# Kernel optimization log

Measured on AMD Instinct MI355X. Metric: run time of the kernel, lower is better.

## Reference

```python
import jax, jax.numpy as jnp
import numpy as np
import math

D = 128  # hidden_dim
N_USERS = 10000
N_ITEMS = 12000
NEG_INF = -9e15


def setup_inputs() -> dict:
    key = jax.random.key(0)
    k1, k2, k3, k4, k5 = jax.random.split(key, 5)
    ufea = jax.random.normal(k1, (N_USERS, D), dtype=jnp.float32)
    inter = jax.random.normal(k2, (N_ITEMS, D), dtype=jnp.float32)
    adj = jax.random.randint(k3, (N_USERS, N_ITEMS), 0, 2, dtype=jnp.int32)
    # linear layer params (torch default init approximated with scaled normals)
    W = jax.random.normal(k4, (D, D), dtype=jnp.float32) / jnp.sqrt(jnp.float32(D))
    b = jax.random.normal(k5, (D,), dtype=jnp.float32) * 0.01
    return {"ufea": ufea, "inter": inter, "adj": adj, "W": W, "b": b}


def _leaky_relu2(x):
    # nn.LeakyReLU(2): negative_slope = 2
    return jnp.where(x > 0, x, 2.0 * x)


def reference(ufea, inter, adj, W, b):
    # GAT.forward_user with dropout in eval mode (identity).
    # Attention.forward(a=ufea, b=inter, adj)
    query = ufea @ W.T + b                      # [N, D]  nn.Linear
    scale = 1.0 / math.sqrt(D)
    scores = _leaky_relu2((query @ inter.T) * scale)   # [N, M]
    scores = jnp.where(adj > 0, scores, NEG_INF)        # mask non-edges
    attn = jax.nn.softmax(scores, axis=1)               # row softmax
    result = attn @ inter                                # [N, D]
    return result
```

## Files before the change

kernel.cpp:

```cpp
#include <hip/hip_runtime.h>
#include <cstdint>
#include <cstddef>


#define N_USERS 10000
#define N_ITEMS 12000
#define HD      128
#define QROWS   10112
#define NCHUNK  16
#define TILE    64
#define NTILES  188
#define UBLOCKS 79
#define QBLOCKS 632

typedef __bf16 bf16x8 __attribute__((ext_vector_type(8)));
typedef __bf16 bf16x4 __attribute__((ext_vector_type(4)));
typedef float  f32x4  __attribute__((ext_vector_type(4)));
typedef int    i32x4  __attribute__((ext_vector_type(4)));

typedef const __attribute__((address_space(1))) unsigned int g_u32;
typedef __attribute__((address_space(3))) unsigned int l_u32;

__global__ __launch_bounds__(256) void cast_inter_kernel(const float* __restrict__ inter,
                                                         __bf16* __restrict__ kvg) {
    __shared__ __bf16 Tl[128 * 72];
    const int t  = threadIdx.x;
    const int tile = blockIdx.x;
    const int i0 = tile * 64;
    for (int it = 0; it < 8; ++it) {
        int g   = it * 256 + t;
        int row = g >> 5;
        int d   = (g & 31) * 4;
        int item = i0 + row;
        if (item < N_ITEMS) {
            f32x4 v = *(const f32x4*)(inter + (size_t)item * HD + d);
            Tl[(d + 0) * 72 + row] = (__bf16)v.x;
            Tl[(d + 1) * 72 + row] = (__bf16)v.y;
            Tl[(d + 2) * 72 + row] = (__bf16)v.z;
            Tl[(d + 3) * 72 + row] = (__bf16)v.w;
        } else {
            Tl[(d + 0) * 72 + row] = (__bf16)0.f;
            Tl[(d + 1) * 72 + row] = (__bf16)0.f;
            Tl[(d + 2) * 72 + row] = (__bf16)0.f;
            Tl[(d + 3) * 72 + row] = (__bf16)0.f;
        }
    }
    __syncthreads();
    const int lane = t & 63, wave = t >> 6;
    const int n = lane & 15, qd = lane >> 4;
    __bf16* tbase = kvg + (size_t)tile * (32 * 512);
    #pragma unroll
    for (int j = 0; j < 4; ++j) {
        const int c = wave * 4 + j;
        int row = i0 + 4 * n + wave;
        bf16x8 o;
        if (row < N_ITEMS) {
            const float* p = inter + (size_t)row * HD + j * 32 + qd * 8;
            f32x4 lo = *(const f32x4*)p, hi = *(const f32x4*)(p + 4);
            o[0]=(__bf16)lo.x; o[1]=(__bf16)lo.y; o[2]=(__bf16)lo.z; o[3]=(__bf16)lo.w;
            o[4]=(__bf16)hi.x; o[5]=(__bf16)hi.y; o[6]=(__bf16)hi.z; o[7]=(__bf16)hi.w;
        } else {
            #pragma unroll
            for (int e = 0; e < 8; ++e) o[e] = (__bf16)0.f;
        }
        *(bf16x8*)(tbase + (size_t)c * 512 + lane * 8) = o;
    }
    #pragma unroll
    for (int j = 0; j < 4; ++j) {
        const int cc = wave * 4 + j;
        const int dt = cc >> 1, kc = cc & 1;
        bf16x8 v = *(const bf16x8*)&Tl[(dt * 16 + n) * 72 + kc * 32 + qd * 8];
        *(bf16x8*)(tbase + (size_t)(16 + cc) * 512 + lane * 8) = v;
    }
}

__global__ __launch_bounds__(256) void query_kernel(const float* __restrict__ ufea,
                                                    const float* __restrict__ W,
                                                    const float* __restrict__ bias,
                                                    __bf16* __restrict__ qg) {
    const int lane = threadIdx.x & 63, wave = threadIdx.x >> 6;
    const int n = lane & 15, qd = lane >> 4;
    const int user0 = blockIdx.x * 16;
    int arow = user0 + n; if (arow > N_USERS - 1) arow = N_USERS - 1;

    bf16x8 af[4];
    #pragma unroll
    for (int kk = 0; kk < 4; ++kk) {
        const float* p = ufea + (size_t)arow * HD + kk * 32 + qd * 8;
        f32x4 lo = *(const f32x4*)p, hi = *(const f32x4*)(p + 4);
        bf16x8 a;
        a[0]=(__bf16)lo.x; a[1]=(__bf16)lo.y; a[2]=(__bf16)lo.z; a[3]=(__bf16)lo.w;
        a[4]=(__bf16)hi.x; a[5]=(__bf16)hi.y; a[6]=(__bf16)hi.z; a[7]=(__bf16)hi.w;
        af[kk] = a;
    }
    #pragma unroll
    for (int h = 0; h < 2; ++h) {
        const int nt = wave * 2 + h;
        f32x4 acc = {0.f, 0.f, 0.f, 0.f};
        #pragma unroll
        for (int kk = 0; kk < 4; ++kk) {
            const float* p = W + (size_t)(nt * 16 + n) * HD + kk * 32 + qd * 8;
            f32x4 lo = *(const f32x4*)p, hi = *(const f32x4*)(p + 4);
            bf16x8 b;
            b[0]=(__bf16)lo.x; b[1]=(__bf16)lo.y; b[2]=(__bf16)lo.z; b[3]=(__bf16)lo.w;
            b[4]=(__bf16)hi.x; b[5]=(__bf16)hi.y; b[6]=(__bf16)hi.z; b[7]=(__bf16)hi.w;
            acc = __builtin_amdgcn_mfma_f32_16x16x32_bf16(af[kk], b, acc, 0, 0, 0);
        }
        const float bv = bias[nt * 16 + n];
        #pragma unroll
        for (int r = 0; r < 4; ++r) {
            int row = user0 + qd * 4 + r;
            qg[(size_t)row * HD + nt * 16 + n] = (__bf16)(acc[r] + bv);
        }
    }
}

__global__ __launch_bounds__(256, 2) void fused_kernel(const __bf16* __restrict__ qg,
                                                       const __bf16* __restrict__ kvg,
                                                       const int* __restrict__ adj,
                                                       float* __restrict__ Opart,
                                                       float* __restrict__ lpart) {
    __shared__ __bf16 Kbuf[16 * 512];
    __shared__ __bf16 Vbuf[16 * 512];
    __shared__ __bf16 Pl[4][32 * 72];
    const int lane = threadIdx.x & 63, wave = threadIdx.x >> 6;
    const int n = lane & 15, qd = lane >> 4;
    const int user0 = blockIdx.y * 128 + wave * 32;
    const int chunk = blockIdx.x;
    const int t0 = (chunk * NTILES) / NCHUNK;
    const int t1 = ((chunk + 1) * NTILES) / NCHUNK;
    const float SC = (float)(1.4426950408889634 * 0.08838834764831845);

    bf16x8 qf[2][4];
    #pragma unroll
    for (int g = 0; g < 2; ++g)
        #pragma unroll
        for (int kk = 0; kk < 4; ++kk)
            qf[g][kk] = *(const bf16x8*)(qg + (size_t)(user0 + g * 16 + n) * HD + kk * 32 + qd * 8);

    f32x4 Oacc[2][8];
    #pragma unroll
    for (int g = 0; g < 2; ++g)
        #pragma unroll
        for (int dt = 0; dt < 8; ++dt) Oacc[g][dt] = (f32x4){0.f, 0.f, 0.f, 0.f};
    float lacc[2][4] = {{0.f,0.f,0.f,0.f},{0.f,0.f,0.f,0.f}};

    int adjOff[2][4];
    #pragma unroll
    for (int g = 0; g < 2; ++g)
        #pragma unroll
        for (int r = 0; r < 4; ++r) {
            int u = user0 + g * 16 + qd * 4 + r;
            if (u > N_USERS - 1) u = N_USERS - 1;
            adjOff[g][r] = u * N_ITEMS;
        }
    __bf16* pw = &Pl[wave][0];

    i32x4 avA[2][4], avB[2][4];
    {
        int col4 = t0 * TILE + 4 * n;
        if (col4 > N_ITEMS - 4) col4 = N_ITEMS - 4;
        #pragma unroll
        for (int g = 0; g < 2; ++g)
            #pragma unroll
            for (int r = 0; r < 4; ++r)
                avA[g][r] = __builtin_nontemporal_load((const i32x4*)(adj + adjOff[g][r] + col4));
    }

    auto tile_iter = [&](int T, i32x4 (&avu)[2][4], i32x4 (&avp)[2][4]) {
        const int j0 = T * TILE;
        __syncthreads();

        #pragma unroll
        for (int j = 0; j < 4; ++j) {
            const int c = wave * 4 + j;
            const __bf16* src = kvg + ((size_t)T * 32 + c) * 512 + lane * 8;
            __builtin_amdgcn_global_load_lds((g_u32*)src, (l_u32*)(&Kbuf[c * 512]), 16, 0, 0);
        }
        #pragma unroll
        for (int j = 0; j < 4; ++j) {
            const int c = wave * 4 + j;
            const __bf16* src = kvg + ((size_t)T * 32 + 16 + c) * 512 + lane * 8;
            __builtin_amdgcn_global_load_lds((g_u32*)src, (l_u32*)(&Vbuf[c * 512]), 16, 0, 0);
        }
        __syncthreads();

        {
            int tn = T + 1; if (tn > t1 - 1) tn = t1 - 1;
            int col4 = tn * TILE + 4 * n;
            if (col4 > N_ITEMS - 4) col4 = N_ITEMS - 4;
            #pragma unroll
            for (int g = 0; g < 2; ++g)
                #pragma unroll
                for (int r = 0; r < 4; ++r)
                    avp[g][r] = __builtin_nontemporal_load((const i32x4*)(adj + adjOff[g][r] + col4));
        }

        f32x4 S[2][4];
        #pragma unroll
        for (int g = 0; g < 2; ++g)
            #pragma unroll
            for (int nt = 0; nt < 4; ++nt) S[g][nt] = (f32x4){0.f, 0.f, 0.f, 0.f};
        #pragma unroll
        for (int nt = 0; nt < 4; ++nt) {
            #pragma unroll
            for (int kk = 0; kk < 4; ++kk) {
                bf16x8 b = *(const bf16x8*)(&Kbuf[(nt * 4 + kk) * 512 + lane * 8]);
                S[0][nt] = __builtin_amdgcn_mfma_f32_16x16x32_bf16(qf[0][kk], b, S[0][nt], 0, 0, 0);
                S[1][nt] = __builtin_amdgcn_mfma_f32_16x16x32_bf16(qf[1][kk], b, S[1][nt], 0, 0, 0);
            }
        }
        #pragma unroll
        for (int g = 0; g < 2; ++g) {
            #pragma unroll
            for (int r = 0; r < 4; ++r) {
                bf16x4 pk;
                #pragma unroll
                for (int nt = 0; nt < 4; ++nt) {
                    float s = S[g][nt][r] * SC;
                    s = fminf(s, s + s);
                    const bool on = (j0 + 4 * n + nt < N_ITEMS) && (avu[g][r][nt] > 0);
                    float p = on ? __builtin_amdgcn_exp2f(s) : 0.f;
                    lacc[g][r] += p;
                    pk[nt] = (__bf16)p;
                }
                *(bf16x4*)(pw + (g * 16 + qd * 4 + r) * 72 + 4 * n) = pk;
            }
        }
        #pragma unroll
        for (int kc = 0; kc < 2; ++kc) {
            bf16x8 af0 = *(const bf16x8*)(pw + (0 * 16 + n) * 72 + kc * 32 + qd * 8);
            bf16x8 af1 = *(const bf16x8*)(pw + (1 * 16 + n) * 72 + kc * 32 + qd * 8);
            #pragma unroll
            for (int dt = 0; dt < 8; ++dt) {
                bf16x8 b = *(const bf16x8*)(&Vbuf[(dt * 2 + kc) * 512 + lane * 8]);
                Oacc[0][dt] = __builtin_amdgcn_mfma_f32_16x16x32_bf16(af0, b, Oacc[0][dt], 0, 0, 0);
                Oacc[1][dt] = __builtin_amdgcn_mfma_f32_16x16x32_bf16(af1, b, Oacc[1][dt], 0, 0, 0);
            }
        }
    };

    int t = t0;
    while (true) {
        tile_iter(t, avA, avB); ++t; if (t >= t1) break;
        tile_iter(t, avB, avA); ++t; if (t >= t1) break;
    }

    #pragma unroll
    for (int g = 0; g < 2; ++g)
        #pragma unroll
        for (int r = 0; r < 4; ++r) {
            float v = lacc[g][r];
            v += __shfl_xor(v, 1);
            v += __shfl_xor(v, 2);
            v += __shfl_xor(v, 4);
            v += __shfl_xor(v, 8);
            lacc[g][r] = v;
        }
    const size_t cb = (size_t)chunk * QROWS;
    #pragma unroll
    for (int g = 0; g < 2; ++g)
        #pragma unroll
        for (int r = 0; r < 4; ++r) {
            const int user = user0 + g * 16 + qd * 4 + r;
            if (user < N_USERS) {
                #pragma unroll
                for (int dt = 0; dt < 8; ++dt)
                    Opart[(cb + user) * HD + dt * 16 + n] = Oacc[g][dt][r];
                if (n == 0) lpart[cb + user] = lacc[g][r];
            }
        }
}

__global__ __launch_bounds__(256) void combine_kernel(const float* __restrict__ Opart,
                                                      const float* __restrict__ lpart,
                                                      float* __restrict__ out) {
    const int g = blockIdx.x * 256 + threadIdx.x;
    const int base = g * 4;
    const int user = base >> 7;
    const int d = base & 127;
    f32x4 acc = {0.f, 0.f, 0.f, 0.f};
    float l = 0.f;
    #pragma unroll
    for (int c = 0; c < NCHUNK; ++c) {
        acc += *(const f32x4*)(Opart + ((size_t)c * QROWS + user) * HD + d);
        l += lpart[(size_t)c * QROWS + user];
    }
    if (user < N_USERS) {
        f32x4 res = acc / l;
        *(f32x4*)(out + (size_t)user * HD + d) = res;
    }
}

extern "C" void kernel_launch(void* const* d_in, const int* in_sizes, int n_in,
                              void* d_out, int out_size, void* d_ws, size_t ws_size,
                              hipStream_t stream) {
    const float* ufea = (const float*)d_in[0];
    const float* inter = (const float*)d_in[1];
    const int*   adj  = (const int*)d_in[2];
    const float* W    = (const float*)d_in[3];
    const float* bias = (const float*)d_in[4];
    float* out = (float*)d_out;

    char* ws = (char*)d_ws;
    __bf16* kvg  = (__bf16*)(ws);
    __bf16* qg   = (__bf16*)(ws + 6160384);
    float*  Opart = (float*)(ws + 8749056);
    float*  lpart = (float*)(ws + 91586560);

    cast_inter_kernel<<<dim3(NTILES), dim3(256), 0, stream>>>(inter, kvg);
    query_kernel<<<dim3(QBLOCKS), dim3(256), 0, stream>>>(ufea, W, bias, qg);
    fused_kernel<<<dim3(NCHUNK, UBLOCKS), dim3(256), 0, stream>>>(qg, kvg, adj, Opart, lpart);
    combine_kernel<<<dim3(1264), dim3(256), 0, stream>>>(Opart, lpart, out);
}
```

Baseline: 689.9 us.

## Double-buffer K tiles, merge prep kernels, and reduce chunk count

Merges the inter-cast and query-projection kernels into one launch, which removes one kernel launch and the gap between them. Double-buffers the K tile in LDS and prefetches the next tile's K during compute, while loading the next V after the PV matmul, so global-to-LDS latency overlaps with MFMA work. Lowers the item-chunk split from 16 to 12, which shrinks the partial-output workspace and the combine work but leaves fewer blocks in the fused grid. Extra LDS for the second K buffer may lower occupancy, and the combine kernel must also be using the new chunk count.

```diff
diff --git a/kernel.cpp b/kernel.cpp
--- a/kernel.cpp
+++ b/kernel.cpp
@@ -7,7 +7,7 @@
 #define N_ITEMS 12000
 #define HD      128
 #define QROWS   10112
-#define NCHUNK  16
+#define NCHUNK  12
 #define TILE    64
 #define NTILES  188
 #define UBLOCKS 79
@@ -21,96 +21,96 @@
 typedef const __attribute__((address_space(1))) unsigned int g_u32;
 typedef __attribute__((address_space(3))) unsigned int l_u32;
 
-__global__ __launch_bounds__(256) void cast_inter_kernel(const float* __restrict__ inter,
-                                                         __bf16* __restrict__ kvg) {
+__global__ __launch_bounds__(256) void prep_kernel(const float* __restrict__ inter,
+                                                   const float* __restrict__ ufea,
+                                                   const float* __restrict__ W,
+                                                   const float* __restrict__ bias,
+                                                   __bf16* __restrict__ kvg,
+                                                   __bf16* __restrict__ qg) {
     __shared__ __bf16 Tl[128 * 72];
-    const int t  = threadIdx.x;
-    const int tile = blockIdx.x;
-    const int i0 = tile * 64;
-    for (int it = 0; it < 8; ++it) {
-        int g   = it * 256 + t;
-        int row = g >> 5;
-        int d   = (g & 31) * 4;
-        int item = i0 + row;
-        if (item < N_ITEMS) {
-            f32x4 v = *(const f32x4*)(inter + (size_t)item * HD + d);
-            Tl[(d + 0) * 72 + row] = (__bf16)v.x;
-            Tl[(d + 1) * 72 + row] = (__bf16)v.y;
-            Tl[(d + 2) * 72 + row] = (__bf16)v.z;
-            Tl[(d + 3) * 72 + row] = (__bf16)v.w;
-        } else {
-            Tl[(d + 0) * 72 + row] = (__bf16)0.f;
-            Tl[(d + 1) * 72 + row] = (__bf16)0.f;
-            Tl[(d + 2) * 72 + row] = (__bf16)0.f;
-            Tl[(d + 3) * 72 + row] = (__bf16)0.f;
-        }
-    }
-    __syncthreads();
+    const int t = threadIdx.x;
     const int lane = t & 63, wave = t >> 6;
     const int n = lane & 15, qd = lane >> 4;
-    __bf16* tbase = kvg + (size_t)tile * (32 * 512);
-    #pragma unroll
-    for (int j = 0; j < 4; ++j) {
-        const int c = wave * 4 + j;
-        int row = i0 + 4 * n + wave;
-        bf16x8 o;
-        if (row < N_ITEMS) {
-            const float* p = inter + (size_t)row * HD + j * 32 + qd * 8;
+
+    if (blockIdx.x < NTILES) {
+        const int tile = blockIdx.x;
+        const int i0 = tile * 64;
+        for (int it = 0; it < 8; ++it) {
+            int g   = it * 256 + t;
+            int row = g >> 5;
+            int d   = (g & 31) * 4;
+            int item = i0 + row;
+            if (item < N_ITEMS) {
+                f32x4 v = *(const f32x4*)(inter + (size_t)item * HD + d);
+                Tl[(d + 0) * 72 + row] = (__bf16)v.x;
+                Tl[(d + 1) * 72 + row] = (__bf16)v.y;
+                Tl[(d + 2) * 72 + row] = (__bf16)v.z;
+                Tl[(d + 3) * 72 + row] = (__bf16)v.w;
+            } else {
+                Tl[(d + 0) * 72 + row] = (__bf16)0.f;
+                Tl[(d + 1) * 72 + row] = (__bf16)0.f;
+                Tl[(d + 2) * 72 + row] = (__bf16)0.f;
+                Tl[(d + 3) * 72 + row] = (__bf16)0.f;
+            }
+        }
+        __syncthreads();
+        __bf16* tbase = kvg + (size_t)tile * (32 * 512);
+        #pragma unroll
+        for (int j = 0; j < 4; ++j) {
+            const int c = wave * 4 + j;
+            int row = i0 + 4 * n + wave;
+            bf16x8 o;
+            if (row < N_ITEMS) {
+                const float* p = inter + (size_t)row * HD + j * 32 + qd * 8;
+                f32x4 lo = *(const f32x4*)p, hi = *(const f32x4*)(p + 4);
+                o[0]=(__bf16)lo.x; o[1]=(__bf16)lo.y; o[2]=(__bf16)lo.z; o[3]=(__bf16)lo.w;
+                o[4]=(__bf16)hi.x; o[5]=(__bf16)hi.y; o[6]=(__bf16)hi.z; o[7]=(__bf16)hi.w;
+            } else {
+                #pragma unroll
+                for (int e = 0; e < 8; ++e) o[e] = (__bf16)0.f;
+            }
+            *(bf16x8*)(tbase + (size_t)c * 512 + lane * 8) = o;
+        }
+        #pragma unroll
+        for (int j = 0; j < 4; ++j) {
+            const int cc = wave * 4 + j;
+            const int dt = cc >> 1, kc = cc & 1;
+            bf16x8 v = *(const bf16x8*)&Tl[(dt * 16 + n) * 72 + kc * 32 + qd * 8];
+            *(bf16x8*)(tbase + (size_t)(16 + cc) * 512 + lane * 8) = v;
+        }
+    } else {
+        const int user0 = (blockIdx.x - NTILES) * 16;
+        int arow = user0 + n; if (arow > N_USERS - 1) arow = N_USERS - 1;
+
+        bf16x8 af[4];
+        #pragma unroll
+        for (int kk = 0; kk < 4; ++kk) {
+            const float* p = ufea + (size_t)arow * HD + kk * 32 + qd * 8;
             f32x4 lo = *(const f32x4*)p, hi = *(const f32x4*)(p + 4);
-            o[0]=(__bf16)lo.x; o[1]=(__bf16)lo.y; o[2]=(__bf16)lo.z; o[3]=(__bf16)lo.w;
-            o[4]=(__bf16)hi.x; o[5]=(__bf16)hi.y; o[6]=(__bf16)hi.z; o[7]=(__bf16)hi.w;
-        } else {
-            #pragma unroll
-            for (int e = 0; e < 8; ++e) o[e] = (__bf16)0.f;
-        }
-        *(bf16x8*)(tbase + (size_t)c * 512 + lane * 8) = o;
-    }
-    #pragma unroll
-    for (int j = 0; j < 4; ++j) {
-        const int cc = wave * 4 + j;
-        const int dt = cc >> 1, kc = cc & 1;
-        bf16x8 v = *(const bf16x8*)&Tl[(dt * 16 + n) * 72 + kc * 32 + qd * 8];
-        *(bf16x8*)(tbase + (size_t)(16 + cc) * 512 + lane * 8) = v;
-    }
-}
-
-__global__ __launch_bounds__(256) void query_kernel(const float* __restrict__ ufea,
-                                                    const float* __restrict__ W,
-                                                    const float* __restrict__ bias,
-                                                    __bf16* __restrict__ qg) {
-    const int lane = threadIdx.x & 63, wave = threadIdx.x >> 6;
-    const int n = lane & 15, qd = lane >> 4;
-    const int user0 = blockIdx.x * 16;
-    int arow = user0 + n; if (arow > N_USERS - 1) arow = N_USERS - 1;
-
-    bf16x8 af[4];
-    #pragma unroll
-    for (int kk = 0; kk < 4; ++kk) {
-        const float* p = ufea + (size_t)arow * HD + kk * 32 + qd * 8;
-        f32x4 lo = *(const f32x4*)p, hi = *(const f32x4*)(p + 4);
-        bf16x8 a;
-        a[0]=(__bf16)lo.x; a[1]=(__bf16)lo.y; a[2]=(__bf16)lo.z; a[3]=(__bf16)lo.w;
-        a[4]=(__bf16)hi.x; a[5]=(__bf16)hi.y; a[6]=(__bf16)hi.z; a[7]=(__bf16)hi.w;
-        af[kk] = a;
-    }
-    #pragma unroll
-    for (int h = 0; h < 2; ++h) {
-        const int nt = wave * 2 + h;
-        f32x4 acc = {0.f, 0.f, 0.f, 0.f};
-        #pragma unroll
-        for (int kk = 0; kk < 4; ++kk) {
-            const float* p = W + (size_t)(nt * 16 + n) * HD + kk * 32 + qd * 8;
-            f32x4 lo = *(const f32x4*)p, hi = *(const f32x4*)(p + 4);
-            bf16x8 b;
-            b[0]=(__bf16)lo.x; b[1]=(__bf16)lo.y; b[2]=(__bf16)lo.z; b[3]=(__bf16)lo.w;
-            b[4]=(__bf16)hi.x; b[5]=(__bf16)hi.y; b[6]=(__bf16)hi.z; b[7]=(__bf16)hi.w;
-            acc = __builtin_amdgcn_mfma_f32_16x16x32_bf16(af[kk], b, acc, 0, 0, 0);
-        }
-        const float bv = bias[nt * 16 + n];
-        #pragma unroll
-        for (int r = 0; r < 4; ++r) {
-            int row = user0 + qd * 4 + r;
-            qg[(size_t)row * HD + nt * 16 + n] = (__bf16)(acc[r] + bv);
+            bf16x8 a;
+            a[0]=(__bf16)lo.x; a[1]=(__bf16)lo.y; a[2]=(__bf16)lo.z; a[3]=(__bf16)lo.w;
+            a[4]=(__bf16)hi.x; a[5]=(__bf16)hi.y; a[6]=(__bf16)hi.z; a[7]=(__bf16)hi.w;
+            af[kk] = a;
+        }
+        #pragma unroll
+        for (int h = 0; h < 2; ++h) {
+            const int nt = wave * 2 + h;
+            f32x4 acc = {0.f, 0.f, 0.f, 0.f};
+            #pragma unroll
+            for (int kk = 0; kk < 4; ++kk) {
+                const float* p = W + (size_t)(nt * 16 + n) * HD + kk * 32 + qd * 8;
+                f32x4 lo = *(const f32x4*)p, hi = *(const f32x4*)(p + 4);
+                bf16x8 b;
+                b[0]=(__bf16)lo.x; b[1]=(__bf16)lo.y; b[2]=(__bf16)lo.z; b[3]=(__bf16)lo.w;
+                b[4]=(__bf16)hi.x; b[5]=(__bf16)hi.y; b[6]=(__bf16)hi.z; b[7]=(__bf16)hi.w;
+                acc = __builtin_amdgcn_mfma_f32_16x16x32_bf16(af[kk], b, acc, 0, 0, 0);
+            }
+            const float bv = bias[nt * 16 + n];
+            #pragma unroll
+            for (int r = 0; r < 4; ++r) {
+                int row = user0 + qd * 4 + r;
+                qg[(size_t)row * HD + nt * 16 + n] = (__bf16)(acc[r] + bv);
+            }
         }
     }
 }
@@ -120,7 +120,7 @@
                                                        const int* __restrict__ adj,
                                                        float* __restrict__ Opart,
                                                        float* __restrict__ lpart) {
-    __shared__ __bf16 Kbuf[16 * 512];
+    __shared__ __bf16 Kbuf[2][16 * 512];
     __shared__ __bf16 Vbuf[16 * 512];
     __shared__ __bf16 Pl[4][32 * 72];
     const int lane = threadIdx.x & 63, wave = threadIdx.x >> 6;
@@ -158,6 +158,19 @@
 
     i32x4 avA[2][4], avB[2][4];
     {
+        const __bf16* tb = kvg + (size_t)t0 * (32 * 512);
+        #pragma unroll
+        for (int j = 0; j < 4; ++j) {
+            const int c = wave * 4 + j;
+            __builtin_amdgcn_global_load_lds((g_u32*)(tb + (size_t)c * 512 + lane * 8),
+                                             (l_u32*)(&Kbuf[0][c * 512]), 16, 0, 0);
+        }
+        #pragma unroll
+        for (int j = 0; j < 4; ++j) {
+            const int c = wave * 4 + j;
+            __builtin_amdgcn_global_load_lds((g_u32*)(tb + (size_t)(16 + c) * 512 + lane * 8),
+                                             (l_u32*)(&Vbuf[c * 512]), 16, 0, 0);
+        }
         int col4 = t0 * TILE + 4 * n;
         if (col4 > N_ITEMS - 4) col4 = N_ITEMS - 4;
         #pragma unroll
@@ -166,25 +179,21 @@
             for (int r = 0; r < 4; ++r)
                 avA[g][r] = __builtin_nontemporal_load((const i32x4*)(adj + adjOff[g][r] + col4));
     }
-
-    auto tile_iter = [&](int T, i32x4 (&avu)[2][4], i32x4 (&avp)[2][4]) {
+    __syncthreads();
+
+    auto tile_iter = [&](int T, int cur, i32x4 (&avu)[2][4], i32x4 (&avp)[2][4]) {
         const int j0 = T * TILE;
-        __syncthreads();
-
-        #pragma unroll
-        for (int j = 0; j < 4; ++j) {
-            const int c = wave * 4 + j;
-            const __bf16* src = kvg + ((size_t)T * 32 + c) * 512 + lane * 8;
-            __builtin_amdgcn_global_load_lds((g_u32*)src, (l_u32*)(&Kbuf[c * 512]), 16, 0, 0);
-        }
-        #pragma unroll
-        for (int j = 0; j < 4; ++j) {
-            const int c = wave * 4 + j;
-            const __bf16* src = kvg + ((size_t)T * 32 + 16 + c) * 512 + lane * 8;
-            __builtin_amdgcn_global_load_lds((g_u32*)src, (l_u32*)(&Vbuf[c * 512]), 16, 0, 0);
-        }
-        __syncthreads();
-
+        const bool more = (T + 1 < t1);
+        const __bf16* tbn = kvg + (size_t)(T + 1) * (32 * 512);
+
+        if (more) {
+            #pragma unroll
+            for (int j = 0; j < 4; ++j) {
+                const int c = wave * 4 + j;
+                __builtin_amdgcn_global_load_lds((g_u32*)(tbn + (size_t)c * 512 + lane * 8),
+                                                 (l_u32*)(&Kbuf[cur ^ 1][c * 512]), 16, 0, 0);
+            }
+        }
         {
             int tn = T + 1; if (tn > t1 - 1) tn = t1 - 1;
             int col4 = tn * TILE + 4 * n;
@@ -201,15 +210,17 @@
         for (int g = 0; g < 2; ++g)
             #pragma unroll
             for (int nt = 0; nt < 4; ++nt) S[g][nt] = (f32x4){0.f, 0.f, 0.f, 0.f};
+        const __bf16* kb = &Kbuf[cur][0];
         #pragma unroll
         for (int nt = 0; nt < 4; ++nt) {
             #pragma unroll
             for (int kk = 0; kk < 4; ++kk) {
-                bf16x8 b = *(const bf16x8*)(&Kbuf[(nt * 4 + kk) * 512 + lane * 8]);
+                bf16x8 b = *(const bf16x8*)(kb + (nt * 4 + kk) * 512 + lane * 8);
                 S[0][nt] = __builtin_amdgcn_mfma_f32_16x16x32_bf16(qf[0][kk], b, S[0][nt], 0, 0, 0);
                 S[1][nt] = __builtin_amdgcn_mfma_f32_16x16x32_bf16(qf[1][kk], b, S[1][nt], 0, 0, 0);
             }
         }
+
         #pragma unroll
         for (int g = 0; g < 2; ++g) {
             #pragma unroll
@@ -227,6 +238,9 @@
                 *(bf16x4*)(pw + (g * 16 + qd * 4 + r) * 72 + 4 * n) = pk;
             }
         }
+
+        __syncthreads();
+
         #pragma unroll
         for (int kc = 0; kc < 2; ++kc) {
             bf16x8 af0 = *(const bf16x8*)(pw + (0 * 16 + n) * 72 + kc * 32 + qd * 8);
@@ -238,12 +252,23 @@
                 Oacc[1][dt] = __builtin_amdgcn_mfma_f32_16x16x32_bf16(af1, b, Oacc[1][dt], 0, 0, 0);
             }
         }
+
+        __syncthreads();
+
+        if (more) {
+            #pragma unroll
+            for (int j = 0; j < 4; ++j) {
+                const int c = wave * 4 + j;
+                __builtin_amdgcn_global_load_lds((g_u32*)(tbn + (size_t)(16 + c) * 512 + lane * 8),
+                                                 (l_u32*)(&Vbuf[c * 512]), 16, 0, 0);
+            }
+        }
     };
 
-    int t = t0;
+    int T = t0;
     while (true) {
-        tile_iter(t, avA, avB); ++t; if (t >= t1) break;
-        tile_iter(t, avB, avA); ++t; if (t >= t1) break;
+        tile_iter(T, 0, avA, avB); ++T; if (T >= t1) break;
+        tile_iter(T, 1, avB, avA); ++T; if (T >= t1) break;
     }
 
     #pragma unroll
@@ -306,10 +331,9 @@
     __bf16* kvg  = (__bf16*)(ws);
     __bf16* qg   = (__bf16*)(ws + 6160384);
     float*  Opart = (float*)(ws + 8749056);
-    float*  lpart = (float*)(ws + 91586560);
-
-    cast_inter_kernel<<<dim3(NTILES), dim3(256), 0, stream>>>(inter, kvg);
-    query_kernel<<<dim3(QBLOCKS), dim3(256), 0, stream>>>(ufea, W, bias, qg);
+    float*  lpart = (float*)(ws + 70877184);
+
+    prep_kernel<<<dim3(NTILES + QBLOCKS), dim3(256), 0, stream>>>(inter, ufea, W, bias, kvg, qg);
     fused_kernel<<<dim3(NCHUNK, UBLOCKS), dim3(256), 0, stream>>>(qg, kvg, adj, Opart, lpart);
     combine_kernel<<<dim3(1264), dim3(256), 0, stream>>>(Opart, lpart, out);
 }
```

Result: faster. 663.9 us (-3.8%).
